# Kernel optimization log

Measured on AMD Instinct MI355X. Metric: run time of the kernel, lower is better.

Reference implementation:

```python
import jax, jax.numpy as jnp
import numpy as np

D_MODEL = 2048
NUM_HEADS = 16
HEAD_DIM = D_MODEL // NUM_HEADS
SCALE = 1.0 / np.sqrt(HEAD_DIM).astype(np.float32)
NEG_INF = -1e9


def setup_inputs() -> dict:
    key = jax.random.key(0)
    ks = jax.random.split(key, 10)
    B, S = 2, 2048
    x = jax.random.normal(ks[0], (B, S, D_MODEL), dtype=jnp.float32)
    # causal lower-triangular mask, broadcastable over (B, H)
    causal_mask = jnp.tril(jnp.ones((S, S), dtype=jnp.int32))[None, None]
    init = 1.0 / np.sqrt(D_MODEL)
    def lin(kw, kb):
        W = jax.random.uniform(kw, (D_MODEL, D_MODEL), jnp.float32, -init, init)
        b = jax.random.uniform(kb, (D_MODEL,), jnp.float32, -init, init)
        return W, b
    Wq, bq = lin(ks[1], ks[2])
    Wk, bk = lin(ks[3], ks[4])
    Wv, bv = lin(ks[5], ks[6])
    Wo, bo = lin(ks[7], ks[8])
    return {"x": x, "causal_mask": causal_mask,
            "Wq": Wq, "bq": bq, "Wk": Wk, "bk": bk,
            "Wv": Wv, "bv": bv, "Wo": Wo, "bo": bo}


def reference(x, causal_mask, Wq, bq, Wk, bk, Wv, bv, Wo, bo):
    B, S, _ = x.shape
    def proj(W, b):
        # torch Linear: x @ W.T + b -> (B, H, S, Dh)
        y = jnp.einsum('bsd,ed->bse', x, W) + b
        return y.reshape(B, S, NUM_HEADS, HEAD_DIM).transpose(0, 2, 1, 3)
    q = proj(Wq, bq)
    k = proj(Wk, bk)
    v = proj(Wv, bv)
    # apply_rope is a no-op stub in the source; q, k unchanged.
    scores = jnp.einsum('bhqd,bhkd->bhqk', q, k) * SCALE
    scores = jnp.where(causal_mask == 0, NEG_INF, scores)
    attn = jax.nn.softmax(scores, axis=-1)
    out = jnp.einsum('bhqk,bhkd->bhqd', attn, v)
    out = out.transpose(0, 2, 1, 3).reshape(B, S, D_MODEL)
    return jnp.einsum('bsd,ed->bse', out, Wo) + bo
```

## Files before the change

### kernel.cpp

```cpp
#include <hip/hip_runtime.h>
#include <hip/hip_bf16.h>
#include <stdint.h>
#include <stddef.h>

typedef __bf16 bf16_t;
typedef __bf16 bf16x4_t __attribute__((ext_vector_type(4)));
typedef __bf16 bf16x8_t __attribute__((ext_vector_type(8)));
typedef float f32x4 __attribute__((ext_vector_type(4)));

#define D_MODEL 2048
#define NHEADS 16
#define HDIM 128
#define SEQ 2048
#define BATCH 2
#define MTOT (BATCH * SEQ)
#define SCALE_F 0.08838834764831845f
#define LOG2E 1.4426950408889634f

#define AS1 __attribute__((address_space(1)))
#define AS3 __attribute__((address_space(3)))

__device__ __forceinline__ void load_lds16(const bf16_t* g, bf16_t* l) {
  __builtin_amdgcn_global_load_lds((AS1 void*)(g), (AS3 void*)(l), 16, 0, 0);
}

__global__ void cast_kernel(const float* __restrict__ src, bf16_t* __restrict__ dst, int n4) {
  int i = blockIdx.x * blockDim.x + threadIdx.x;
  if (i < n4) {
    float4 v = ((const float4*)src)[i];
    bf16x4_t o;
    o.x = (bf16_t)v.x; o.y = (bf16_t)v.y; o.z = (bf16_t)v.z; o.w = (bf16_t)v.w;
    ((bf16x4_t*)dst)[i] = o;
  }
}

__global__ void cast4_kernel(const float* __restrict__ s0, const float* __restrict__ s1,
                             const float* __restrict__ s2, const float* __restrict__ s3,
                             bf16_t* __restrict__ dst, int n4) {
  int i = blockIdx.x * blockDim.x + threadIdx.x;
  int y = blockIdx.y;
  if (i < n4) {
    const float* src = (y == 0) ? s0 : (y == 1) ? s1 : (y == 2) ? s2 : s3;
    float4 v = ((const float4*)src)[i];
    bf16x4_t o;
    o.x = (bf16_t)v.x; o.y = (bf16_t)v.y; o.z = (bf16_t)v.z; o.w = (bf16_t)v.w;
    ((bf16x4_t*)(dst + (size_t)y * D_MODEL * D_MODEL / 4 * 4))[i] = o;
  }
}

__global__ __launch_bounds__(256) void gemm_fused(
    const bf16_t* __restrict__ A, const bf16_t* __restrict__ Bm, int mode,
    const float* __restrict__ bias0, const float* __restrict__ bias1,
    const float* __restrict__ bias2,
    bf16_t* __restrict__ Qo, bf16_t* __restrict__ Ko, bf16_t* __restrict__ Vto,
    float* __restrict__ Out) {
  const int K = 2048;
  __shared__ __align__(16) bf16_t lA[128 * 64];
  __shared__ __align__(16) bf16_t lB[128 * 64];
  const int m0 = blockIdx.x * 128;
  const int n0 = blockIdx.y * 128;
  const int t = threadIdx.x;
  const int w = t >> 6, lane = t & 63;
  const int wm = w & 1, wn = w >> 1;
  const int la = lane & 15, lb = lane >> 4;

  f32x4 acc[4][4];
  f32x4 zero = {0.f, 0.f, 0.f, 0.f};
#pragma unroll
  for (int i = 0; i < 4; i++)
#pragma unroll
    for (int j = 0; j < 4; j++) acc[i][j] = zero;

  const int row0 = t >> 3, cc = t & 7;
  const int ccs = cc ^ (row0 & 7);
  const bf16_t* gA = A + (size_t)(m0 + row0) * K + ccs * 8;
  const bf16_t* gB = Bm + (size_t)(n0 + row0) * K + ccs * 8;
  bf16_t* sA = lA + t * 8;
  bf16_t* sB = lB + t * 8;

  for (int k0 = 0; k0 < K; k0 += 64) {
    __syncthreads();
#pragma unroll
    for (int i = 0; i < 4; i++)
      load_lds16(gA + k0 + (size_t)(32 * i) * K, sA + 2048 * i);
#pragma unroll
    for (int i = 0; i < 4; i++)
      load_lds16(gB + k0 + (size_t)(32 * i) * K, sB + 2048 * i);
    __syncthreads();
#pragma unroll
    for (int ks = 0; ks < 2; ks++) {
      bf16x8_t af[4], bfr[4];
#pragma unroll
      for (int mt = 0; mt < 4; mt++) {
        int row = wm * 64 + mt * 16 + la;
        af[mt] = *(const bf16x8_t*)(lA + row * 64 + (((ks * 4 + lb) ^ (la & 7)) * 8));
      }
#pragma unroll
      for (int nt = 0; nt < 4; nt++) {
        int row = wn * 64 + nt * 16 + la;
        bfr[nt] = *(const bf16x8_t*)(lB + row * 64 + (((ks * 4 + lb) ^ (la & 7)) * 8));
      }
#pragma unroll
      for (int mt = 0; mt < 4; mt++)
#pragma unroll
        for (int nt = 0; nt < 4; nt++)
          acc[mt][nt] = __builtin_amdgcn_mfma_f32_16x16x32_bf16(af[mt], bfr[nt], acc[mt][nt], 0, 0, 0);
    }
  }

  if (mode == 0) {
#pragma unroll
    for (int mt = 0; mt < 4; mt++) {
#pragma unroll
      for (int nt = 0; nt < 4; nt++) {
        int m = m0 + wm * 64 + mt * 16 + lb * 4;
        int n = n0 + wn * 64 + nt * 16 + la;
        int b = m >> 11, s = m & 2047;
        int which = n >> 11, hd = n & 2047;
        int h = hd >> 7, d = hd & 127;
        float bv = (which == 0 ? bias0 : which == 1 ? bias1 : bias2)[hd];
        f32x4 v = acc[mt][nt];
        if (which == 2) {
          bf16_t* dst = Vto + ((size_t)(b * NHEADS + h) * HDIM + d) * SEQ + s;
          bf16x4_t pk;
          pk.x = (bf16_t)(v.x + bv); pk.y = (bf16_t)(v.y + bv);
          pk.z = (bf16_t)(v.z + bv); pk.w = (bf16_t)(v.w + bv);
          *(bf16x4_t*)dst = pk;
        } else {
          bf16_t* dst = (which == 0 ? Qo : Ko) + ((size_t)(b * NHEADS + h) * SEQ + s) * HDIM + d;
          dst[0]        = (bf16_t)(v.x + bv);
          dst[HDIM]     = (bf16_t)(v.y + bv);
          dst[2 * HDIM] = (bf16_t)(v.z + bv);
          dst[3 * HDIM] = (bf16_t)(v.w + bv);
        }
      }
    }
  } else {
#pragma unroll
    for (int mt = 0; mt < 4; mt++) {
#pragma unroll
      for (int nt = 0; nt < 4; nt++) {
        int m = m0 + wm * 64 + mt * 16 + lb * 4;
        int n = n0 + wn * 64 + nt * 16 + la;
        float bv = bias0[n];
        f32x4 v = acc[mt][nt];
        float* dst = Out + (size_t)m * D_MODEL + n;
        dst[0]           = v.x + bv;
        dst[D_MODEL]     = v.y + bv;
        dst[2 * D_MODEL] = v.z + bv;
        dst[3 * D_MODEL] = v.w + bv;
      }
    }
  }
}

__global__ __launch_bounds__(256) void flash_attn(
    const bf16_t* __restrict__ Q, const bf16_t* __restrict__ Kg,
    const bf16_t* __restrict__ Vt, bf16_t* __restrict__ O) {
  __shared__ __align__(16) bf16_t lK[64 * 128];
  __shared__ __align__(16) bf16_t lV[128 * 64];
  __shared__ __align__(16) bf16_t lP[128 * 72];
  int g = blockIdx.x;
  int qt, bh;
  if (g < 256) { qt = g >> 5; bh = g & 31; }
  else         { qt = 15 - ((g - 256) >> 5); bh = g & 31; }
  const int q0 = qt * 128;
  const int t = threadIdx.x;
  const int w = t >> 6, lane = t & 63;
  const int la = lane & 15, lb = lane >> 4;

  const bf16_t* Qb = Q + (size_t)bh * SEQ * HDIM;
  const bf16_t* Kb = Kg + (size_t)bh * SEQ * HDIM;
  const bf16_t* Vb = Vt + (size_t)bh * HDIM * SEQ;

  bf16x8_t qf[2][4];
#pragma unroll
  for (int mt = 0; mt < 2; mt++)
#pragma unroll
    for (int ks = 0; ks < 4; ks++)
      qf[mt][ks] = *(const bf16x8_t*)(Qb + (size_t)(q0 + w * 32 + mt * 16 + la) * HDIM + ks * 32 + lb * 8);

  f32x4 oacc[2][8];
  float mrow[2][4], lrow[2][4];
  f32x4 zero = {0.f, 0.f, 0.f, 0.f};
#pragma unroll
  for (int mt = 0; mt < 2; mt++) {
#pragma unroll
    for (int dt = 0; dt < 8; dt++) oacc[mt][dt] = zero;
#pragma unroll
    for (int r = 0; r < 4; r++) { mrow[mt][r] = -3.0e38f; lrow[mt][r] = 0.f; }
  }

  const float scale2 = SCALE_F * LOG2E;
  const int nkt = qt * 2 + 2;
  for (int kt = 0; kt < nkt; kt++) {
    const int j0 = kt * 64;
    __syncthreads();
#pragma unroll
    for (int i = 0; i < 4; i++) {
      int slot = t + 256 * i;
      int j = slot >> 4, cc = slot & 15;
      load_lds16(Kb + (size_t)(j0 + j) * HDIM + ((cc ^ (j & 15)) * 8), lK + slot * 8);
    }
#pragma unroll
    for (int i = 0; i < 4; i++) {
      int slot = t + 256 * i;
      int d = slot >> 3, jc = slot & 7;
      load_lds16(Vb + (size_t)d * SEQ + j0 + ((jc ^ (d & 7)) * 8), lV + slot * 8);
    }
    __syncthreads();

    f32x4 sacc[2][4];
#pragma unroll
    for (int mt = 0; mt < 2; mt++)
#pragma unroll
      for (int nt = 0; nt < 4; nt++) sacc[mt][nt] = zero;
#pragma unroll
    for (int ks = 0; ks < 4; ks++) {
#pragma unroll
      for (int nt = 0; nt < 4; nt++) {
        int j = nt * 16 + la;
        int cc = (lb + 4 * ks) ^ (j & 15);
        bf16x8_t kf = *(const bf16x8_t*)(lK + j * 128 + cc * 8);
#pragma unroll
        for (int mt = 0; mt < 2; mt++)
          sacc[mt][nt] = __builtin_amdgcn_mfma_f32_16x16x32_bf16(qf[mt][ks], kf, sacc[mt][nt], 0, 0, 0);
      }
    }

#pragma unroll
    for (int mt = 0; mt < 2; mt++) {
      int qrow = q0 + w * 32 + mt * 16 + lb * 4;
      f32x4 rmax;
#pragma unroll
      for (int r = 0; r < 4; r++) {
        float x = -3.0e38f;
#pragma unroll
        for (int nt = 0; nt < 4; nt++) {
          int j = j0 + nt * 16 + la;
          float sv = sacc[mt][nt][r] * scale2;
          if (j > qrow + r) sv = -3.0e38f;
          sacc[mt][nt][r] = sv;
          x = fmaxf(x, sv);
        }
        rmax[r] = x;
      }
#pragma unroll
      for (int off = 1; off < 16; off <<= 1)
#pragma unroll
        for (int r = 0; r < 4; r++) rmax[r] = fmaxf(rmax[r], __shfl_xor(rmax[r], off));
      f32x4 rsum;
#pragma unroll
      for (int r = 0; r < 4; r++) {
        float mnew = fmaxf(mrow[mt][r], rmax[r]);
        float alpha = exp2f(mrow[mt][r] - mnew);
        mrow[mt][r] = mnew;
        lrow[mt][r] *= alpha;
#pragma unroll
        for (int dt = 0; dt < 8; dt++) oacc[mt][dt][r] *= alpha;
        float s = 0.f;
#pragma unroll
        for (int nt = 0; nt < 4; nt++) {
          float pex = exp2f(sacc[mt][nt][r] - mnew);
          sacc[mt][nt][r] = pex;
          s += pex;
        }
        rsum[r] = s;
      }
#pragma unroll
      for (int off = 1; off < 16; off <<= 1)
#pragma unroll
        for (int r = 0; r < 4; r++) rsum[r] += __shfl_xor(rsum[r], off);
#pragma unroll
      for (int r = 0; r < 4; r++) lrow[mt][r] += rsum[r];
#pragma unroll
      for (int nt = 0; nt < 4; nt++)
#pragma unroll
        for (int r = 0; r < 4; r++)
          lP[(w * 32 + mt * 16 + lb * 4 + r) * 72 + nt * 16 + la] = (bf16_t)sacc[mt][nt][r];
    }

    bf16x8_t pf[2][2];
#pragma unroll
    for (int mt = 0; mt < 2; mt++)
#pragma unroll
      for (int ks = 0; ks < 2; ks++)
        pf[mt][ks] = *(const bf16x8_t*)(lP + (w * 32 + mt * 16 + la) * 72 + ks * 32 + lb * 8);
#pragma unroll
    for (int ks = 0; ks < 2; ks++) {
#pragma unroll
      for (int dt = 0; dt < 8; dt++) {
        int d = dt * 16 + la;
        int jc = (lb + 4 * ks) ^ (d & 7);
        bf16x8_t vf = *(const bf16x8_t*)(lV + d * 64 + jc * 8);
#pragma unroll
        for (int mt = 0; mt < 2; mt++)
          oacc[mt][dt] = __builtin_amdgcn_mfma_f32_16x16x32_bf16(pf[mt][ks], vf, oacc[mt][dt], 0, 0, 0);
      }
    }
  }

  const int b = bh >> 4, h = bh & 15;
#pragma unroll
  for (int mt = 0; mt < 2; mt++) {
    f32x4 inv;
#pragma unroll
    for (int r = 0; r < 4; r++) inv[r] = 1.0f / lrow[mt][r];
#pragma unroll
    for (int dt = 0; dt < 8; dt++) {
#pragma unroll
      for (int r = 0; r < 4; r++) {
        int q = q0 + w * 32 + mt * 16 + lb * 4 + r;
        int d = h * HDIM + dt * 16 + la;
        O[((size_t)b * SEQ + q) * D_MODEL + d] = (bf16_t)(oacc[mt][dt][r] * inv[r]);
      }
    }
  }
}

extern "C" void kernel_launch(void* const* d_in, const int* in_sizes, int n_in,
                              void* d_out, int out_size, void* d_ws, size_t ws_size,
                              hipStream_t stream) {
  (void)in_sizes; (void)n_in; (void)out_size; (void)ws_size;
  const float* x  = (const float*)d_in[0];
  const float* Wq = (const float*)d_in[2];
  const float* bq = (const float*)d_in[3];
  const float* Wk = (const float*)d_in[4];
  const float* bk = (const float*)d_in[5];
  const float* Wv = (const float*)d_in[6];
  const float* bv = (const float*)d_in[7];
  const float* Wo = (const float*)d_in[8];
  const float* bo = (const float*)d_in[9];
  float* out = (float*)d_out;

  const size_t NBF = (size_t)MTOT * D_MODEL * sizeof(bf16_t);
  const size_t WBF = (size_t)D_MODEL * D_MODEL * sizeof(bf16_t);
  char* p = (char*)d_ws;
  bf16_t* xb   = (bf16_t*)p; p += NBF;
  bf16_t* Wcat = (bf16_t*)p; p += 4 * WBF;
  bf16_t* Qb   = (bf16_t*)p; p += NBF;
  bf16_t* Kb   = (bf16_t*)p; p += NBF;
  bf16_t* Vtb  = (bf16_t*)p; p += NBF;
  bf16_t* Wob  = Wcat + (size_t)3 * D_MODEL * D_MODEL;
  bf16_t* Ob   = xb;

  const int WN4 = D_MODEL * D_MODEL / 4;
  const int XN4 = MTOT * D_MODEL / 4;
  cast_kernel<<<XN4 / 256, 256, 0, stream>>>(x, xb, XN4);
  cast4_kernel<<<dim3(WN4 / 256, 4), 256, 0, stream>>>(Wq, Wk, Wv, Wo, Wcat, WN4);

  gemm_fused<<<dim3(MTOT / 128, 6144 / 128), 256, 0, stream>>>(
      xb, Wcat, 0, bq, bk, bv, Qb, Kb, Vtb, nullptr);

  flash_attn<<<dim3(512), 256, 0, stream>>>(Qb, Kb, Vtb, Ob);

  gemm_fused<<<dim3(MTOT / 128, D_MODEL / 128), 256, 0, stream>>>(
      Ob, Wob, 1, bo, nullptr, nullptr, nullptr, nullptr, nullptr, out);
}
```

Before: 415.7 us.

## Split long causal query tiles across two blocks and merge partial softmax results

```diff
diff --git a/kernel.cpp b/kernel.cpp
--- a/kernel.cpp
+++ b/kernel.cpp
@@ -16,6 +16,7 @@
 #define MTOT (BATCH * SEQ)
 #define SCALE_F 0.08838834764831845f
 #define LOG2E 1.4426950408889634f
+#define QSCALE (SCALE_F * LOG2E)
 
 #define AS1 __attribute__((address_space(1)))
 #define AS3 __attribute__((address_space(3)))
@@ -127,11 +128,12 @@
           pk.z = (bf16_t)(v.z + bv); pk.w = (bf16_t)(v.w + bv);
           *(bf16x4_t*)dst = pk;
         } else {
+          float sc = (which == 0) ? QSCALE : 1.0f;
           bf16_t* dst = (which == 0 ? Qo : Ko) + ((size_t)(b * NHEADS + h) * SEQ + s) * HDIM + d;
-          dst[0]        = (bf16_t)(v.x + bv);
-          dst[HDIM]     = (bf16_t)(v.y + bv);
-          dst[2 * HDIM] = (bf16_t)(v.z + bv);
-          dst[3 * HDIM] = (bf16_t)(v.w + bv);
+          dst[0]        = (bf16_t)((v.x + bv) * sc);
+          dst[HDIM]     = (bf16_t)((v.y + bv) * sc);
+          dst[2 * HDIM] = (bf16_t)((v.z + bv) * sc);
+          dst[3 * HDIM] = (bf16_t)((v.w + bv) * sc);
         }
       }
     }
@@ -154,20 +156,30 @@
   }
 }
 
-__global__ __launch_bounds__(256) void flash_attn(
+__global__ __launch_bounds__(256, 3) void flash_attn(
     const bf16_t* __restrict__ Q, const bf16_t* __restrict__ Kg,
-    const bf16_t* __restrict__ Vt, bf16_t* __restrict__ O) {
+    const bf16_t* __restrict__ Vt, bf16_t* __restrict__ O,
+    bf16_t* __restrict__ PO, float* __restrict__ ML) {
   __shared__ __align__(16) bf16_t lK[64 * 128];
   __shared__ __align__(16) bf16_t lV[128 * 64];
   __shared__ __align__(16) bf16_t lP[128 * 72];
-  int g = blockIdx.x;
-  int qt, bh;
-  if (g < 256) { qt = g >> 5; bh = g & 31; }
-  else         { qt = 15 - ((g - 256) >> 5); bh = g & 31; }
+  const int g = blockIdx.x;
+  const int piece = g >> 5, bh = g & 31;
+  int qt, kt0, kt1, half;
+  bool partial;
+  if (piece < 16) {
+    qt = 8 + (piece >> 1); half = piece & 1; partial = true;
+    kt0 = half ? (qt + 1) : 0;
+    kt1 = half ? (2 * qt + 2) : (qt + 1);
+  } else {
+    qt = piece - 16; half = 0; partial = false;
+    kt0 = 0; kt1 = 2 * qt + 2;
+  }
   const int q0 = qt * 128;
   const int t = threadIdx.x;
   const int w = t >> 6, lane = t & 63;
   const int la = lane & 15, lb = lane >> 4;
+  const int qloc = w * 32 + la;
 
   const bf16_t* Qb = Q + (size_t)bh * SEQ * HDIM;
   const bf16_t* Kb = Kg + (size_t)bh * SEQ * HDIM;
@@ -178,22 +190,17 @@
   for (int mt = 0; mt < 2; mt++)
 #pragma unroll
     for (int ks = 0; ks < 4; ks++)
-      qf[mt][ks] = *(const bf16x8_t*)(Qb + (size_t)(q0 + w * 32 + mt * 16 + la) * HDIM + ks * 32 + lb * 8);
+      qf[mt][ks] = *(const bf16x8_t*)(Qb + (size_t)(q0 + qloc + mt * 16) * HDIM + ks * 32 + lb * 8);
 
   f32x4 oacc[2][8];
-  float mrow[2][4], lrow[2][4];
+  float mr[2] = {-3.0e38f, -3.0e38f}, lr[2] = {0.f, 0.f};
   f32x4 zero = {0.f, 0.f, 0.f, 0.f};
 #pragma unroll
-  for (int mt = 0; mt < 2; mt++) {
+  for (int mt = 0; mt < 2; mt++)
 #pragma unroll
     for (int dt = 0; dt < 8; dt++) oacc[mt][dt] = zero;
-#pragma unroll
-    for (int r = 0; r < 4; r++) { mrow[mt][r] = -3.0e38f; lrow[mt][r] = 0.f; }
-  }
-
-  const float scale2 = SCALE_F * LOG2E;
-  const int nkt = qt * 2 + 2;
-  for (int kt = 0; kt < nkt; kt++) {
+
+  for (int kt = kt0; kt < kt1; kt++) {
     const int j0 = kt * 64;
     __syncthreads();
 #pragma unroll
@@ -210,11 +217,11 @@
     }
     __syncthreads();
 
-    f32x4 sacc[2][4];
-#pragma unroll
-    for (int mt = 0; mt < 2; mt++)
-#pragma unroll
-      for (int nt = 0; nt < 4; nt++) sacc[mt][nt] = zero;
+    f32x4 st[4][2];
+#pragma unroll
+    for (int nt = 0; nt < 4; nt++)
+#pragma unroll
+      for (int mt = 0; mt < 2; mt++) st[nt][mt] = zero;
 #pragma unroll
     for (int ks = 0; ks < 4; ks++) {
 #pragma unroll
@@ -224,60 +231,50 @@
         bf16x8_t kf = *(const bf16x8_t*)(lK + j * 128 + cc * 8);
 #pragma unroll
         for (int mt = 0; mt < 2; mt++)
-          sacc[mt][nt] = __builtin_amdgcn_mfma_f32_16x16x32_bf16(qf[mt][ks], kf, sacc[mt][nt], 0, 0, 0);
-      }
-    }
-
+          st[nt][mt] = __builtin_amdgcn_mfma_f32_16x16x32_bf16(kf, qf[mt][ks], st[nt][mt], 0, 0, 0);
+      }
+    }
+
+    const bool dm = (j0 + 64 > q0);
 #pragma unroll
     for (int mt = 0; mt < 2; mt++) {
-      int qrow = q0 + w * 32 + mt * 16 + lb * 4;
-      f32x4 rmax;
-#pragma unroll
-      for (int r = 0; r < 4; r++) {
-        float x = -3.0e38f;
-#pragma unroll
-        for (int nt = 0; nt < 4; nt++) {
-          int j = j0 + nt * 16 + la;
-          float sv = sacc[mt][nt][r] * scale2;
-          if (j > qrow + r) sv = -3.0e38f;
-          sacc[mt][nt][r] = sv;
-          x = fmaxf(x, sv);
+      int qg = q0 + qloc + mt * 16;
+      if (dm) {
+#pragma unroll
+        for (int nt = 0; nt < 4; nt++)
+#pragma unroll
+          for (int r = 0; r < 4; r++)
+            if (j0 + nt * 16 + lb * 4 + r > qg) st[nt][mt][r] = -3.0e38f;
+      }
+      float tm = -3.0e38f;
+#pragma unroll
+      for (int nt = 0; nt < 4; nt++)
+#pragma unroll
+        for (int r = 0; r < 4; r++) tm = fmaxf(tm, st[nt][mt][r]);
+      tm = fmaxf(tm, __shfl_xor(tm, 16));
+      tm = fmaxf(tm, __shfl_xor(tm, 32));
+      float mnew = fmaxf(mr[mt], tm);
+      float alpha = exp2f(mr[mt] - mnew);
+      mr[mt] = mnew;
+      lr[mt] *= alpha;
+#pragma unroll
+      for (int dt = 0; dt < 8; dt++) oacc[mt][dt] *= alpha;
+      float s = 0.f;
+#pragma unroll
+      for (int nt = 0; nt < 4; nt++) {
+        f32x4 p;
+#pragma unroll
+        for (int r = 0; r < 4; r++) {
+          p[r] = exp2f(st[nt][mt][r] - mnew);
+          s += p[r];
         }
-        rmax[r] = x;
-      }
-#pragma unroll
-      for (int off = 1; off < 16; off <<= 1)
-#pragma unroll
-        for (int r = 0; r < 4; r++) rmax[r] = fmaxf(rmax[r], __shfl_xor(rmax[r], off));
-      f32x4 rsum;
-#pragma unroll
-      for (int r = 0; r < 4; r++) {
-        float mnew = fmaxf(mrow[mt][r], rmax[r]);
-        float alpha = exp2f(mrow[mt][r] - mnew);
-        mrow[mt][r] = mnew;
-        lrow[mt][r] *= alpha;
-#pragma unroll
-        for (int dt = 0; dt < 8; dt++) oacc[mt][dt][r] *= alpha;
-        float s = 0.f;
-#pragma unroll
-        for (int nt = 0; nt < 4; nt++) {
-          float pex = exp2f(sacc[mt][nt][r] - mnew);
-          sacc[mt][nt][r] = pex;
-          s += pex;
-        }
-        rsum[r] = s;
-      }
-#pragma unroll
-      for (int off = 1; off < 16; off <<= 1)
-#pragma unroll
-        for (int r = 0; r < 4; r++) rsum[r] += __shfl_xor(rsum[r], off);
-#pragma unroll
-      for (int r = 0; r < 4; r++) lrow[mt][r] += rsum[r];
-#pragma unroll
-      for (int nt = 0; nt < 4; nt++)
-#pragma unroll
-        for (int r = 0; r < 4; r++)
-          lP[(w * 32 + mt * 16 + lb * 4 + r) * 72 + nt * 16 + la] = (bf16_t)sacc[mt][nt][r];
+        bf16x4_t pk;
+        pk.x = (bf16_t)p[0]; pk.y = (bf16_t)p[1]; pk.z = (bf16_t)p[2]; pk.w = (bf16_t)p[3];
+        *(bf16x4_t*)(lP + (qloc + mt * 16) * 72 + nt * 16 + lb * 4) = pk;
+      }
+      s += __shfl_xor(s, 16);
+      s += __shfl_xor(s, 32);
+      lr[mt] += s;
     }
 
     bf16x8_t pf[2][2];
@@ -285,7 +282,7 @@
     for (int mt = 0; mt < 2; mt++)
 #pragma unroll
       for (int ks = 0; ks < 2; ks++)
-        pf[mt][ks] = *(const bf16x8_t*)(lP + (w * 32 + mt * 16 + la) * 72 + ks * 32 + lb * 8);
+        pf[mt][ks] = *(const bf16x8_t*)(lP + (qloc + mt * 16) * 72 + ks * 32 + lb * 8);
 #pragma unroll
     for (int ks = 0; ks < 2; ks++) {
 #pragma unroll
@@ -295,26 +292,77 @@
         bf16x8_t vf = *(const bf16x8_t*)(lV + d * 64 + jc * 8);
 #pragma unroll
         for (int mt = 0; mt < 2; mt++)
-          oacc[mt][dt] = __builtin_amdgcn_mfma_f32_16x16x32_bf16(pf[mt][ks], vf, oacc[mt][dt], 0, 0, 0);
-      }
-    }
-  }
-
+          oacc[mt][dt] = __builtin_amdgcn_mfma_f32_16x16x32_bf16(vf, pf[mt][ks], oacc[mt][dt], 0, 0, 0);
+      }
+    }
+  }
+
+  if (!partial) {
+    const int b = bh >> 4, h = bh & 15;
+#pragma unroll
+    for (int mt = 0; mt < 2; mt++) {
+      float inv = 1.0f / lr[mt];
+      int q = q0 + qloc + mt * 16;
+      bf16_t* dst = O + ((size_t)b * SEQ + q) * D_MODEL + h * HDIM + lb * 4;
+#pragma unroll
+      for (int dt = 0; dt < 8; dt++) {
+        f32x4 v = oacc[mt][dt];
+        bf16x4_t pk;
+        pk.x = (bf16_t)(v[0] * inv); pk.y = (bf16_t)(v[1] * inv);
+        pk.z = (bf16_t)(v[2] * inv); pk.w = (bf16_t)(v[3] * inv);
+        *(bf16x4_t*)(dst + dt * 16) = pk;
+      }
+    }
+  } else {
+    const int slot = ((qt - 8) * 32 + bh) * 2 + half;
+    bf16_t* pob = PO + (size_t)slot * 128 * 128;
+#pragma unroll
+    for (int mt = 0; mt < 2; mt++) {
+      int q = qloc + mt * 16;
+      bf16_t* dst = pob + (size_t)q * 128 + lb * 4;
+#pragma unroll
+      for (int dt = 0; dt < 8; dt++) {
+        f32x4 v = oacc[mt][dt];
+        bf16x4_t pk;
+        pk.x = (bf16_t)v[0]; pk.y = (bf16_t)v[1];
+        pk.z = (bf16_t)v[2]; pk.w = (bf16_t)v[3];
+        *(bf16x4_t*)(dst + dt * 16) = pk;
+      }
+      if (lb == 0) {
+        float2 ml = make_float2(mr[mt], lr[mt]);
+        *(float2*)(ML + ((size_t)slot * 128 + q) * 2) = ml;
+      }
+    }
+  }
+}
+
+__global__ void merge_kernel(const bf16_t* __restrict__ PO, const float* __restrict__ ML,
+                             bf16_t* __restrict__ O) {
+  const int qti = blockIdx.x >> 5, bh = blockIdx.x & 31;
+  const int qt = 8 + qti;
+  const int t = threadIdx.x;
+  const int q = t >> 1, dh = (t & 1) * 64;
+  const size_t s1 = ((size_t)(qti * 32 + bh)) * 2;
+  const float* ml1 = ML + (s1 * 128 + q) * 2;
+  const float* ml2 = ML + ((s1 + 1) * 128 + q) * 2;
+  float m1 = ml1[0], l1 = ml1[1], m2 = ml2[0], l2 = ml2[1];
+  float m = fmaxf(m1, m2);
+  float w1 = exp2f(m1 - m), w2 = exp2f(m2 - m);
+  float inv = 1.0f / (w1 * l1 + w2 * l2);
+  w1 *= inv; w2 *= inv;
+  const bf16_t* p1 = PO + (s1 * 128 + q) * 128 + dh;
+  const bf16_t* p2 = PO + ((s1 + 1) * 128 + q) * 128 + dh;
   const int b = bh >> 4, h = bh & 15;
-#pragma unroll
-  for (int mt = 0; mt < 2; mt++) {
-    f32x4 inv;
-#pragma unroll
-    for (int r = 0; r < 4; r++) inv[r] = 1.0f / lrow[mt][r];
-#pragma unroll
-    for (int dt = 0; dt < 8; dt++) {
-#pragma unroll
-      for (int r = 0; r < 4; r++) {
-        int q = q0 + w * 32 + mt * 16 + lb * 4 + r;
-        int d = h * HDIM + dt * 16 + la;
-        O[((size_t)b * SEQ + q) * D_MODEL + d] = (bf16_t)(oacc[mt][dt][r] * inv[r]);
-      }
-    }
+  bf16_t* dst = O + ((size_t)b * SEQ + qt * 128 + q) * D_MODEL + h * HDIM + dh;
+#pragma unroll
+  for (int i = 0; i < 8; i++) {
+    bf16x8_t a = ((const bf16x8_t*)p1)[i];
+    bf16x8_t c = ((const bf16x8_t*)p2)[i];
+    bf16x8_t o;
+#pragma unroll
+    for (int e = 0; e < 8; e++)
+      o[e] = (bf16_t)(w1 * (float)a[e] + w2 * (float)c[e]);
+    ((bf16x8_t*)dst)[i] = o;
   }
 }
 
@@ -343,6 +391,8 @@
   bf16_t* Vtb  = (bf16_t*)p; p += NBF;
   bf16_t* Wob  = Wcat + (size_t)3 * D_MODEL * D_MODEL;
   bf16_t* Ob   = xb;
+  bf16_t* PO = Wcat;
+  float*  ML = (float*)(Wcat + (size_t)512 * 128 * 128);
 
   const int WN4 = D_MODEL * D_MODEL / 4;
   const int XN4 = MTOT * D_MODEL / 4;
@@ -352,7 +402,8 @@
   gemm_fused<<<dim3(MTOT / 128, 6144 / 128), 256, 0, stream>>>(
       xb, Wcat, 0, bq, bk, bv, Qb, Kb, Vtb, nullptr);
 
-  flash_attn<<<dim3(512), 256, 0, stream>>>(Qb, Kb, Vtb, Ob);
+  flash_attn<<<dim3(768), 256, 0, stream>>>(Qb, Kb, Vtb, Ob, PO, ML);
+  merge_kernel<<<dim3(256), 256, 0, stream>>>(PO, ML, Ob);
 
   gemm_fused<<<dim3(MTOT / 128, D_MODEL / 128), 256, 0, stream>>>(
       Ob, Wob, 1, bo, nullptr, nullptr, nullptr, nullptr, nullptr, out);
```

New measurement: 447.3 us. 1.08x slower.
